# Optimization experiments

Hardware: AMD Instinct MI355X
Metric: run time of the kernel (lower is better)

The kernel has to match this reference:

```python
import jax, jax.numpy as jnp
import numpy as np

EPS = 1e-5
NO_ACT = 3

def _causal_conv(x, w, b, dil):
    # x: [B, Cin, T], w: [Cout, Cin, K]; left-pad by (K-1)*dil == Conv1d(pad)+Chomp1d
    pad = (w.shape[2] - 1) * dil
    y = jax.lax.conv_general_dilated(x, w, window_strides=(1,), padding=[(pad, 0)],
                                     rhs_dilation=(dil,), dimension_numbers=("NCH", "OIH", "NCH"))
    return y + b[None, :, None]

def _bn(x, g, bt, m, v):
    # eval-mode BatchNorm1d over channel dim
    return (x - m[None, :, None]) * (g / jnp.sqrt(v + EPS))[None, :, None] + bt[None, :, None]

def _block(x, w1, b1, w2, b2, g1, bt1, m1, v1, g2, bt2, m2, v2, dil, dw=None, db=None):
    out = jax.nn.relu(_bn(_causal_conv(x, w1, b1, dil), g1, bt1, m1, v1))
    out = jax.nn.relu(_bn(_causal_conv(out, w2, b2, dil), g2, bt2, m2, v2))
    res = x if dw is None else _causal_conv(x, dw, db, 1)
    return jax.nn.relu(out + res)

def _logits(x, c0w1, c0b1, c0w2, c0b2, c0g1, c0bt1, c0m1, c0v1, c0g2, c0bt2, c0m2, c0v2, c0dw, c0db,
            c1w1, c1b1, c1w2, c1b2, c1g1, c1bt1, c1m1, c1v1, c1g2, c1bt2, c1m2, c1v2, aw, ab, lw, lb):
    h = jnp.swapaxes(x, 1, 2)  # [B, Cin, T]
    h = _block(h, c0w1, c0b1, c0w2, c0b2, c0g1, c0bt1, c0m1, c0v1, c0g2, c0bt2, c0m2, c0v2, 1, c0dw, c0db)
    h = _block(h, c1w1, c1b1, c1w2, c1b2, c1g1, c1bt1, c1m1, c1v1, c1g2, c1bt2, c1m2, c1v2, 2)
    z = jnp.swapaxes(h, 1, 2)  # [B, T, C]
    attn = jax.nn.sigmoid(z @ aw + ab)  # [B, T, 1]
    return (z * attn) @ lw + lb  # [B, T, 5]

def setup_inputs():
    key = jax.random.key(0)
    ks = iter(jax.random.split(key, 64))
    B, T, CIN, C, K, NC = 32, 4096, 34, 256, 3, 5
    def conv_w(co, ci, k):
        return jax.random.normal(next(ks), (co, ci, k), jnp.float32) * np.float32(np.sqrt(2.0 / (ci * k)))
    def vec(n, kind="randn"):
        if kind == "randn":
            return jax.random.normal(next(ks), (n,), jnp.float32) * 0.1
        return jax.random.uniform(next(ks), (n,), jnp.float32, 0.5, 1.5)
    inp = {"x": jax.random.normal(next(ks), (B, T, CIN), jnp.float32)}
    for i, ci in [(0, CIN), (1, C)]:
        inp[f"c{i}w1"] = conv_w(C, ci, K); inp[f"c{i}b1"] = vec(C)
        inp[f"c{i}w2"] = conv_w(C, C, K); inp[f"c{i}b2"] = vec(C)
        for j in (1, 2):
            inp[f"c{i}g{j}"] = 1.0 + vec(C)
            inp[f"c{i}bt{j}"] = vec(C)
            inp[f"c{i}m{j}"] = vec(C)
            inp[f"c{i}v{j}"] = vec(C, "rand")
    inp["c0dw"] = conv_w(C, CIN, 1); inp["c0db"] = vec(C)
    inp["aw"] = jax.random.normal(next(ks), (C, 1), jnp.float32) * np.float32(np.sqrt(1.0 / C))
    inp["ab"] = vec(1)
    inp["lw"] = jax.random.normal(next(ks), (C, NC), jnp.float32) * np.float32(np.sqrt(1.0 / C))
    inp["lb"] = vec(NC)
    return inp

def reference(x, c0w1, c0b1, c0w2, c0b2, c0g1, c0bt1, c0m1, c0v1, c0g2, c0bt2, c0m2, c0v2, c0dw, c0db,
              c1w1, c1b1, c1w2, c1b2, c1g1, c1bt1, c1m1, c1v1, c1g2, c1bt2, c1m2, c1v2, aw, ab, lw, lb):
    logits = _logits(x, c0w1, c0b1, c0w2, c0b2, c0g1, c0bt1, c0m1, c0v1, c0g2, c0bt2, c0m2, c0v2, c0dw, c0db,
                     c1w1, c1b1, c1w2, c1b2, c1g1, c1bt1, c1m1, c1v1, c1g2, c1bt2, c1m2, c1v2, aw, ab, lw, lb)
    probs = jax.nn.softmax(logits, axis=-1)
    B, T, NC = probs.shape
    preds = jnp.argmax(probs, axis=-1).astype(jnp.int32)
    # --- conservative no-activity: clipped window (size 5) majority check ---
    non3 = (preds != NO_ACT).astype(jnp.int32)
    cs = jnp.concatenate([jnp.zeros((B, 1), jnp.int32), jnp.cumsum(non3, axis=1)], axis=1)  # [B, T+1]
    t = jnp.arange(T)
    start = jnp.maximum(0, t - 2)
    end = jnp.minimum(T, t + 3)
    wsum = cs[:, end] - cs[:, start]          # non-no-activity count in window, [B, T]
    wlen = (end - start)[None, :]
    alt = jnp.argmax(probs.at[:, :, NO_ACT].set(0.0), axis=-1).astype(jnp.int32)
    proc = jnp.where((preds == NO_ACT) & (2 * wsum > wlen), alt, preds)
    # --- transition rules: sequential state smoothing scan over time ---
    TM = jnp.ones((5, 5), jnp.float32).at[1, 2].set(0.0).at[2, 0].set(0.0)
    def step(prev, inp):
        curr, p = inp                          # curr: [B] int32, p: [B, 5]
        mask = TM[prev]                        # allowed next-states, [B, 5]
        invalid = jnp.take_along_axis(mask, curr[:, None], axis=1)[:, 0] == 0
        vp = p * mask
        cand = jnp.where(vp.sum(-1) == 0, prev, jnp.argmax(vp, axis=-1).astype(jnp.int32))
        new = jnp.where(invalid, cand, curr)
        return new, new
    init = proc[:, 0]
    _, rest = jax.lax.scan(step, init, (proc[:, 1:].T, jnp.swapaxes(probs[:, 1:], 0, 1)))
    processed = jnp.concatenate([init[:, None], rest.T], axis=1)  # [B, T]
    return logits, processed
```

## Files before the change

kernel.cpp:

```cpp
#include <hip/hip_runtime.h>
#include <hip/hip_bf16.h>


#define T_LEN 4096
#define CIN   34
#define EPSV  1e-5f
#define HALO  16
#define TT    48
#define TW    64
#define NTILE 86

__device__ __forceinline__ int hswz(int row, int col) {
    return row * TW + ((((col >> 2) ^ ((row >> 3) & 15)) << 2) | (col & 3));
}
__device__ __forceinline__ float4* lds_ptr4(float* buf, int row, int col) {
    return (float4*)&buf[row * TW + (((col >> 2) ^ ((row >> 3) & 15)) << 2)];
}
__device__ __forceinline__ float4 lds_read4(const float* buf, int row, int col) {
    return *(const float4*)&buf[row * TW + (((col >> 2) ^ ((row >> 3) & 15)) << 2)];
}

__device__ __forceinline__ void bs_load(const float* __restrict__ wraw, int ch,
                                        float4 r[3], int tid) {
    #pragma unroll
    for (int k = 0; k < 3; ++k) {
        int s = tid + k * 512;
        int co = s / 6, q = s - co * 6;
        r[k] = *(const float4*)&wraw[co * 768 + ch * 24 + q * 4];
    }
}
__device__ __forceinline__ void bs_write(float* wch, const float4 r[3], int tid) {
    #pragma unroll
    for (int k = 0; k < 3; ++k) {
        int s = tid + k * 512;
        int co = s / 6, q = s - co * 6;
        wch[(q * 4 + 0) * 256 + co] = r[k].x;
        wch[(q * 4 + 1) * 256 + co] = r[k].y;
        wch[(q * 4 + 2) * 256 + co] = r[k].z;
        wch[(q * 4 + 3) * 256 + co] = r[k].w;
    }
}

__device__ __forceinline__ void s1_load(const float* __restrict__ w1, int ch,
                                        float r[12], int tid) {
    int nrows = (ch < 4) ? 24 : 6;
    int slots = nrows * 256;
    #pragma unroll
    for (int k = 0; k < 12; ++k) {
        int s = tid + k * 512;
        if (s < slots) {
            int co = s / nrows, kr = s - co * nrows;
            r[k] = w1[co * 102 + ch * 24 + kr];
        }
    }
}
__device__ __forceinline__ void s1_write(float* wch, int ch, const float r[12], int tid) {
    int nrows = (ch < 4) ? 24 : 6;
    int slots = nrows * 256;
    #pragma unroll
    for (int k = 0; k < 12; ++k) {
        int s = tid + k * 512;
        if (s < slots) {
            int co = s / nrows, kr = s - co * nrows;
            wch[kr * 256 + co] = r[k];
        }
    }
}

__device__ __forceinline__ void ds_stage(float* wch, const float* __restrict__ dw,
                                         int ch, int tid) {
    int nci = (ch < 4) ? 8 : 2;
    int slots = nci * 256;
    #pragma unroll
    for (int k = 0; k < 4; ++k) {
        int s = tid + k * 512;
        if (s < slots) {
            int ci_l = s % nci, co = s / nci;
            wch[ci_l * 256 + co] = dw[co * CIN + ch * 8 + ci_l];
        }
    }
}

template <int DIL>
__device__ __forceinline__ void chunk_compute(const float* src, const float* wch,
                                              int rowBase, int KH, int co0, int c0,
                                              float (&acc)[8][16]) {
    const int cL = (c0 >= 4) ? c0 - 4 : 0;
    #pragma unroll
    for (int rep = 0; rep < 2; ++rep) {
        int ci_l = KH + rep * 4;
        int row = rowBase + ci_l;
        float rw[20];
        *(float4*)&rw[0]  = lds_read4(src, row, cL);
        *(float4*)&rw[4]  = lds_read4(src, row, c0);
        *(float4*)&rw[8]  = lds_read4(src, row, c0 + 4);
        *(float4*)&rw[12] = lds_read4(src, row, c0 + 8);
        *(float4*)&rw[16] = lds_read4(src, row, c0 + 12);
        #pragma unroll
        for (int kk = 0; kk < 3; ++kk) {
            float wv[8];
            *(float4*)&wv[0] = *(const float4*)&wch[(ci_l * 3 + kk) * 256 + co0];
            *(float4*)&wv[4] = *(const float4*)&wch[(ci_l * 3 + kk) * 256 + co0 + 4];
            const int off = (DIL == 2) ? 2 * kk : kk + 2;
            #pragma unroll
            for (int i = 0; i < 8; ++i)
                #pragma unroll
                for (int j = 0; j < 16; ++j)
                    acc[i][j] += wv[i] * rw[j + off];
        }
    }
}

__device__ __forceinline__ void chunk_compute_x(const float* __restrict__ x,
                                                const float* wch, int b, int t0,
                                                int ciBase, int nci, int KH,
                                                int co0, int c0, float (&acc)[8][16]) {
    #pragma unroll
    for (int rep = 0; rep < 2; ++rep) {
        int ci_l = KH + rep * 4;
        if (ci_l < nci) {
            int ci = ciBase + ci_l;
            float rw[20];
            rw[0] = 0.f; rw[1] = 0.f;
            #pragma unroll
            for (int idx = 2; idx < 20; ++idx) {
                int t = t0 - HALO + c0 + idx - 4;
                rw[idx] = (t >= 0 && t < T_LEN) ? x[(b * T_LEN + t) * CIN + ci] : 0.f;
            }
            #pragma unroll
            for (int kk = 0; kk < 3; ++kk) {
                float wv[8];
                *(float4*)&wv[0] = *(const float4*)&wch[(ci_l * 3 + kk) * 256 + co0];
                *(float4*)&wv[4] = *(const float4*)&wch[(ci_l * 3 + kk) * 256 + co0 + 4];
                #pragma unroll
                for (int i = 0; i < 8; ++i)
                    #pragma unroll
                    for (int j = 0; j < 16; ++j)
                        acc[i][j] += wv[i] * rw[j + kk + 2];
            }
        }
    }
}

__device__ __forceinline__ void chunk_compute_ds(const float* __restrict__ x,
                                                 const float* wch, int b, int t0,
                                                 int ciBase, int nci, int KH,
                                                 int co0, int c0, float (&acc)[8][16]) {
    #pragma unroll
    for (int rep = 0; rep < 2; ++rep) {
        int ci_l = KH + rep * 4;
        if (ci_l < nci) {
            int ci = ciBase + ci_l;
            float xv[16];
            #pragma unroll
            for (int j = 0; j < 16; ++j) {
                int t = t0 - HALO + c0 + j;
                xv[j] = (t >= 0 && t < T_LEN) ? x[(b * T_LEN + t) * CIN + ci] : 0.f;
            }
            float wv[8];
            *(float4*)&wv[0] = *(const float4*)&wch[ci_l * 256 + co0];
            *(float4*)&wv[4] = *(const float4*)&wch[ci_l * 256 + co0 + 4];
            #pragma unroll
            for (int i = 0; i < 8; ++i)
                #pragma unroll
                for (int j = 0; j < 16; ++j)
                    acc[i][j] += wv[i] * xv[j];
        }
    }
}

__device__ __forceinline__ void kh_store(float* tgt, float (&acc)[8][16], int co0, int c0) {
    #pragma unroll
    for (int i = 0; i < 8; ++i)
        #pragma unroll
        for (int j4 = 0; j4 < 4; ++j4)
            *lds_ptr4(tgt, co0 + i, c0 + j4 * 4) =
                make_float4(acc[i][j4*4+0], acc[i][j4*4+1], acc[i][j4*4+2], acc[i][j4*4+3]);
}
__device__ __forceinline__ void kh_add(float* tgt, float (&acc)[8][16], int co0, int c0) {
    #pragma unroll
    for (int i = 0; i < 8; ++i)
        #pragma unroll
        for (int j4 = 0; j4 < 4; ++j4) {
            float4* p = lds_ptr4(tgt, co0 + i, c0 + j4 * 4);
            float4 pv = *p;
            pv.x += acc[i][j4*4+0]; pv.y += acc[i][j4*4+1];
            pv.z += acc[i][j4*4+2]; pv.w += acc[i][j4*4+3];
            *p = pv;
        }
}
__device__ __forceinline__ void kh_final0(float* tgt, float (&acc)[8][16],
                                          const float* __restrict__ g,  const float* __restrict__ bt,
                                          const float* __restrict__ m,  const float* __restrict__ v,
                                          const float* __restrict__ bb,
                                          int co0, int c0, int t0) {
    #pragma unroll
    for (int i = 0; i < 8; ++i) {
        int co = co0 + i;
        float sc = g[co] / sqrtf(v[co] + EPSV);
        float bi = (bb[co] - m[co]) * sc + bt[co];
        #pragma unroll
        for (int j4 = 0; j4 < 4; ++j4) {
            float4* p = lds_ptr4(tgt, co, c0 + j4 * 4);
            float4 pv = *p;
            float pr[4] = {pv.x, pv.y, pv.z, pv.w};
            float o[4];
            #pragma unroll
            for (int r = 0; r < 4; ++r) {
                float s = (pr[r] + acc[i][j4*4+r]) * sc + bi;
                o[r] = fmaxf(s, 0.f);
                int t = t0 - HALO + c0 + j4 * 4 + r;
                if (t < 0) o[r] = 0.f;
            }
            *p = make_float4(o[0], o[1], o[2], o[3]);
        }
    }
}
__device__ __forceinline__ void kh_res2(float* tgt, float (&acc)[8][16],
                                        const float* __restrict__ db,
                                        int co0, int c0, int t0) {
    #pragma unroll
    for (int i = 0; i < 8; ++i) {
        float d = db[co0 + i];
        #pragma unroll
        for (int j4 = 0; j4 < 4; ++j4) {
            float4* p = lds_ptr4(tgt, co0 + i, c0 + j4 * 4);
            float4 pv = *p;
            float pr[4] = {pv.x, pv.y, pv.z, pv.w};
            float o[4];
            #pragma unroll
            for (int r = 0; r < 4; ++r) {
                float s = pr[r] + acc[i][j4*4+r] + d;
                o[r] = fmaxf(s, 0.f);
                int t = t0 - HALO + c0 + j4 * 4 + r;
                if (t < 0) o[r] = 0.f;
            }
            *p = make_float4(o[0], o[1], o[2], o[3]);
        }
    }
}

#define ZERO_ACC() { _Pragma("unroll") for (int i = 0; i < 8; ++i) \
                     _Pragma("unroll") for (int j = 0; j < 16; ++j) acc[i][j] = 0.f; }

#define REDUCE0(TGT, G, BT, M, V, BB) {                         \
    __syncthreads();                                            \
    if (KH == 3) kh_store(TGT, acc, co0, c0);                   \
    __syncthreads();                                            \
    if (KH == 2) kh_add(TGT, acc, co0, c0);                     \
    __syncthreads();                                            \
    if (KH == 1) kh_add(TGT, acc, co0, c0);                     \
    __syncthreads();                                            \
    if (KH == 0) kh_final0(TGT, acc, G, BT, M, V, BB, co0, c0, t0); \
    __syncthreads(); }

#define REDUCE_RES(TGT, DB) {                                   \
    __syncthreads();                                            \
    if (KH == 3) kh_add(TGT, acc, co0, c0);                     \
    __syncthreads();                                            \
    if (KH == 2) kh_add(TGT, acc, co0, c0);                     \
    __syncthreads();                                            \
    if (KH == 1) kh_add(TGT, acc, co0, c0);                     \
    __syncthreads();                                            \
    if (KH == 0) kh_res2(TGT, acc, DB, co0, c0, t0);            \
    __syncthreads(); }

__global__ __launch_bounds__(512, 2) void tcn_fused(
    const float* __restrict__ x,
    const float* __restrict__ c0w1, const float* __restrict__ c0b1,
    const float* __restrict__ c0w2, const float* __restrict__ c0b2,
    const float* __restrict__ c0g1, const float* __restrict__ c0bt1,
    const float* __restrict__ c0m1, const float* __restrict__ c0v1,
    const float* __restrict__ c0g2, const float* __restrict__ c0bt2,
    const float* __restrict__ c0m2, const float* __restrict__ c0v2,
    const float* __restrict__ c1w1, const float* __restrict__ c1b1,
    const float* __restrict__ c1w2, const float* __restrict__ c1b2,
    const float* __restrict__ c1g1, const float* __restrict__ c1bt1,
    const float* __restrict__ c1m1, const float* __restrict__ c1v1,
    const float* __restrict__ c1g2, const float* __restrict__ c1bt2,
    const float* __restrict__ c1m2, const float* __restrict__ c1v2,
    const float* __restrict__ c0dw, const float* __restrict__ c0db,
    const float* __restrict__ aw,   const float* __restrict__ ab,
    const float* __restrict__ lw,   const float* __restrict__ lb,
    float* __restrict__ out)
{
    __shared__ float bufA[256 * TW];
    __shared__ float bufB[256 * TW];
    __shared__ float wch[24 * 256];

    const int b   = blockIdx.y;
    const int t0  = blockIdx.x * TT;
    const int tid = threadIdx.x;
    const int CG  = tid & 31, sg = tid >> 5;
    const int TG  = sg & 3,  KH = sg >> 2;
    const int co0 = CG * 8,  c0 = TG * 16;

    float acc[8][16];

    ZERO_ACC();
    {
        float r[12];
        s1_load(c0w1, 0, r, tid);
        for (int ch = 0; ch < 5; ++ch) {
            __syncthreads();
            s1_write(wch, ch, r, tid);
            __syncthreads();
            if (ch + 1 < 5) s1_load(c0w1, ch + 1, r, tid);
            chunk_compute_x(x, wch, b, t0, ch * 8, (ch < 4) ? 8 : 2, KH, co0, c0, acc);
        }
    }
    REDUCE0(bufA, c0g1, c0bt1, c0m1, c0v1, c0b1);

    ZERO_ACC();
    {
        float4 r4[3];
        bs_load(c0w2, 0, r4, tid);
        for (int ch = 0; ch < 32; ++ch) {
            __syncthreads();
            bs_write(wch, r4, tid);
            __syncthreads();
            if (ch + 1 < 32) bs_load(c0w2, ch + 1, r4, tid);
            chunk_compute<1>(bufA, wch, ch * 8, KH, co0, c0, acc);
        }
    }
    REDUCE0(bufB, c0g2, c0bt2, c0m2, c0v2, c0b2);

    ZERO_ACC();
    for (int ch = 0; ch < 5; ++ch) {
        __syncthreads();
        ds_stage(wch, c0dw, ch, tid);
        __syncthreads();
        chunk_compute_ds(x, wch, b, t0, ch * 8, (ch < 4) ? 8 : 2, KH, co0, c0, acc);
    }
    REDUCE_RES(bufB, c0db);

    ZERO_ACC();
    {
        float4 r4[3];
        bs_load(c1w1, 0, r4, tid);
        for (int ch = 0; ch < 32; ++ch) {
            __syncthreads();
            bs_write(wch, r4, tid);
            __syncthreads();
            if (ch + 1 < 32) bs_load(c1w1, ch + 1, r4, tid);
            chunk_compute<2>(bufB, wch, ch * 8, KH, co0, c0, acc);
        }
    }
    REDUCE0(bufA, c1g1, c1bt1, c1m1, c1v1, c1b1);

    ZERO_ACC();
    {
        float4 r4[3];
        bs_load(c1w2, 0, r4, tid);
        for (int ch = 0; ch < 32; ++ch) {
            __syncthreads();
            bs_write(wch, r4, tid);
            __syncthreads();
            if (ch + 1 < 32) bs_load(c1w2, ch + 1, r4, tid);
            chunk_compute<2>(bufA, wch, ch * 8, KH, co0, c0, acc);
        }
    }
    REDUCE0(bufA, c1g2, c1bt2, c1m2, c1v2, c1b2);

    {
        #pragma unroll
        for (int ii = 0; ii < 2; ++ii) {
            int co = co0 + KH * 2 + ii;
            #pragma unroll
            for (int j4 = 0; j4 < 4; ++j4) {
                float4* p = lds_ptr4(bufA, co, c0 + j4 * 4);
                float4 a = *p;
                float4 rr = lds_read4(bufB, co, c0 + j4 * 4);
                a.x = fmaxf(a.x + rr.x, 0.f);
                a.y = fmaxf(a.y + rr.y, 0.f);
                a.z = fmaxf(a.z + rr.z, 0.f);
                a.w = fmaxf(a.w + rr.w, 0.f);
                *p = a;
            }
        }
    }
    __syncthreads();

    for (int s = tid; s < 1542; s += 512) {
        float vput;
        if (s < 256)       vput = aw[s];
        else if (s < 1536) vput = lw[s - 256];
        else if (s == 1536) vput = ab[0];
        else               vput = lb[s - 1537];
        wch[s] = vput;
    }
    __syncthreads();
    {
        int col = tid >> 3, oct = tid & 7;
        if (col >= HALO) {
            int t = t0 - HALO + col;
            float s1 = 0.f, s5[5] = {0.f, 0.f, 0.f, 0.f, 0.f};
            for (int q = 0; q < 32; ++q) {
                int co = oct * 32 + q;
                float z = bufA[hswz(co, col)];
                s1 += z * wch[co];
                #pragma unroll
                for (int nc = 0; nc < 5; ++nc) s5[nc] += z * wch[256 + co * 5 + nc];
            }
            #pragma unroll
            for (int mm = 1; mm <= 4; mm <<= 1) {
                s1 += __shfl_xor(s1, mm, 64);
                #pragma unroll
                for (int nc = 0; nc < 5; ++nc) s5[nc] += __shfl_xor(s5[nc], mm, 64);
            }
            if (oct == 0 && t < T_LEN) {
                float at = 1.f / (1.f + expf(-(s1 + wch[1536])));
                float* dst = &out[(b * T_LEN + t) * 5];
                #pragma unroll
                for (int nc = 0; nc < 5; ++nc) dst[nc] = at * s5[nc] + wch[1537 + nc];
            }
        }
    }
}

__global__ __launch_bounds__(256) void postproc(
    const float* __restrict__ logits, float* __restrict__ outp)
{
    const int b = blockIdx.x;
    const int tid = threadIdx.x;
    __shared__ signed char preds[4096], alt3[4096], ax2[4096], ax0[4096],
                           proc[4096], resa[4096];

    for (int t = tid; t < T_LEN; t += 256) {
        const float* p = &logits[(b * T_LEN + t) * 5];
        float l0 = p[0], l1 = p[1], l2 = p[2], l3 = p[3], l4 = p[4];
        int am = 0; float mv = l0;
        if (l1 > mv) { am = 1; mv = l1; }
        if (l2 > mv) { am = 2; mv = l2; }
        if (l3 > mv) { am = 3; mv = l3; }
        if (l4 > mv) { am = 4; mv = l4; }
        int a3 = 0; float m3 = l0;
        if (l1 > m3) { a3 = 1; m3 = l1; }
        if (l2 > m3) { a3 = 2; m3 = l2; }
        if (l4 > m3) { a3 = 4; }
        int a2 = 0; float m2 = l0;
        if (l1 > m2) { a2 = 1; m2 = l1; }
        if (l3 > m2) { a2 = 3; m2 = l3; }
        if (l4 > m2) { a2 = 4; }
        int a0 = 1; float m0 = l1;
        if (l2 > m0) { a0 = 2; m0 = l2; }
        if (l3 > m0) { a0 = 3; m0 = l3; }
        if (l4 > m0) { a0 = 4; }
        preds[t] = (signed char)am;
        alt3[t]  = (signed char)a3;
        ax2[t]   = (signed char)a2;
        ax0[t]   = (signed char)a0;
    }
    __syncthreads();
    for (int t = tid; t < T_LEN; t += 256) {
        int s0 = t - 2 > 0 ? t - 2 : 0;
        int e0 = t + 3 < T_LEN ? t + 3 : T_LEN;
        int wsum = 0;
        for (int s = s0; s < e0; ++s) wsum += (preds[s] != 3);
        int wl = e0 - s0;
        int pd = preds[t];
        proc[t] = (pd == 3 && 2 * wsum > wl) ? alt3[t] : (signed char)pd;
    }
    __syncthreads();
    if (tid == 0) {
        int p = proc[0];
        resa[0] = (signed char)p;
        for (int t = 1; t < T_LEN; ++t) {
            int c = proc[t];
            int n = c;
            if (p == 1 && c == 2) n = ax2[t];
            else if (p == 2 && c == 0) n = ax0[t];
            resa[t] = (signed char)n;
            p = n;
        }
    }
    __syncthreads();
    for (int t = tid; t < T_LEN; t += 256) outp[b * T_LEN + t] = (float)resa[t];
}

extern "C" void kernel_launch(void* const* d_in, const int* in_sizes, int n_in,
                              void* d_out, int out_size, void* d_ws, size_t ws_size,
                              hipStream_t stream)
{
    const float* x     = (const float*)d_in[0];
    const float* c0w1  = (const float*)d_in[1];
    const float* c0b1  = (const float*)d_in[2];
    const float* c0w2  = (const float*)d_in[3];
    const float* c0b2  = (const float*)d_in[4];
    const float* c0g1  = (const float*)d_in[5];
    const float* c0bt1 = (const float*)d_in[6];
    const float* c0m1  = (const float*)d_in[7];
    const float* c0v1  = (const float*)d_in[8];
    const float* c0g2  = (const float*)d_in[9];
    const float* c0bt2 = (const float*)d_in[10];
    const float* c0m2  = (const float*)d_in[11];
    const float* c0v2  = (const float*)d_in[12];
    const float* c1w1  = (const float*)d_in[13];
    const float* c1b1  = (const float*)d_in[14];
    const float* c1w2  = (const float*)d_in[15];
    const float* c1b2  = (const float*)d_in[16];
    const float* c1g1  = (const float*)d_in[17];
    const float* c1bt1 = (const float*)d_in[18];
    const float* c1m1  = (const float*)d_in[19];
    const float* c1v1  = (const float*)d_in[20];
    const float* c1g2  = (const float*)d_in[21];
    const float* c1bt2 = (const float*)d_in[22];
    const float* c1m2  = (const float*)d_in[23];
    const float* c1v2  = (const float*)d_in[24];
    const float* c0dw  = (const float*)d_in[25];
    const float* c0db  = (const float*)d_in[26];
    const float* aw    = (const float*)d_in[27];
    const float* ab    = (const float*)d_in[28];
    const float* lw    = (const float*)d_in[29];
    const float* lb    = (const float*)d_in[30];

    float* logits = (float*)d_out;

    tcn_fused<<<dim3(NTILE, 32), 512, 0, stream>>>(
        x,
        c0w1, c0b1, c0w2, c0b2,
        c0g1, c0bt1, c0m1, c0v1,
        c0g2, c0bt2, c0m2, c0v2,
        c1w1, c1b1, c1w2, c1b2,
        c1g1, c1bt1, c1m1, c1v1,
        c1g2, c1bt2, c1m2, c1v2,
        c0dw, c0db, aw, ab, lw, lb,
        logits);

    postproc<<<32, 256, 0, stream>>>(logits, ((float*)d_out) + 32 * 4096 * 5);
}
```

Before: 5.066 ms.

## Add prep kernel for transposed weights and 1024-thread fused TCN reading weights from global

A prep kernel transposes all conv weights into a [ci*3+kk][co] layout in the workspace. A new fused kernel then uses 1024 threads, each computing a 4x4 output block, and reads weights straight from global/L2 instead of staging them in LDS. It keeps the activation tile in LDS and splits each channel sweep into four strided partial sums. The intent is to remove the LDS weight staging, the cross-thread LDS reduction barriers and register pressure, at the cost of more global weight traffic and an extra launch.

```diff
diff --git a/kernel.cpp b/kernel.cpp
--- a/kernel.cpp
+++ b/kernel.cpp
@@ -10,6 +10,13 @@
 #define TW    64
 #define NTILE 86
 
+#define WOFF_WT1 0
+#define WOFF_WT2 26112
+#define WOFF_WT3 222720
+#define WOFF_WT4 419328
+#define WOFF_WTD 615936
+#define WS_FLOATS 624640
+
 __device__ __forceinline__ int hswz(int row, int col) {
     return row * TW + ((((col >> 2) ^ ((row >> 3) & 15)) << 2) | (col & 3));
 }
@@ -18,6 +25,301 @@
 }
 __device__ __forceinline__ float4 lds_read4(const float* buf, int row, int col) {
     return *(const float4*)&buf[row * TW + (((col >> 2) ^ ((row >> 3) & 15)) << 2)];
+}
+
+__global__ __launch_bounds__(256) void prep_v3(
+    const float* __restrict__ c0w1, const float* __restrict__ c0w2,
+    const float* __restrict__ c1w1, const float* __restrict__ c1w2,
+    const float* __restrict__ c0dw, float* __restrict__ ws)
+{
+    int idx = blockIdx.x * 256 + threadIdx.x;
+    if (idx < 26112) {
+        int co = idx & 255, r = idx >> 8, ci = r / 3, kk = r % 3;
+        ws[WOFF_WT1 + idx] = c0w1[(co * CIN + ci) * 3 + kk];
+        return;
+    }
+    idx -= 26112;
+    if (idx < 196608) {
+        int co = idx & 255, r = idx >> 8, ci = r / 3, kk = r % 3;
+        ws[WOFF_WT2 + idx] = c0w2[(co * 256 + ci) * 3 + kk];
+        return;
+    }
+    idx -= 196608;
+    if (idx < 196608) {
+        int co = idx & 255, r = idx >> 8, ci = r / 3, kk = r % 3;
+        ws[WOFF_WT3 + idx] = c1w1[(co * 256 + ci) * 3 + kk];
+        return;
+    }
+    idx -= 196608;
+    if (idx < 196608) {
+        int co = idx & 255, r = idx >> 8, ci = r / 3, kk = r % 3;
+        ws[WOFF_WT4 + idx] = c1w2[(co * 256 + ci) * 3 + kk];
+        return;
+    }
+    idx -= 196608;
+    if (idx < 8704) {
+        int co = idx & 255, ci = idx >> 8;
+        ws[WOFF_WTD + idx] = c0dw[co * CIN + ci];
+    }
+}
+
+__device__ __forceinline__ void bzero(float (&bk)[4][4]) {
+    #pragma unroll
+    for (int i = 0; i < 4; ++i)
+        #pragma unroll
+        for (int j = 0; j < 4; ++j) bk[i][j] = 0.f;
+}
+__device__ __forceinline__ void badd(float (&A)[4][4], const float (&B)[4][4]) {
+    #pragma unroll
+    for (int i = 0; i < 4; ++i)
+        #pragma unroll
+        for (int j = 0; j < 4; ++j) A[i][j] = A[i][j] + B[i][j];
+}
+
+__device__ __forceinline__ void sweep_s1(const float* xs, const float* __restrict__ WT,
+                                         int r, int c0, int co0, float (&bk)[4][4]) {
+    bzero(bk);
+    for (int ci = r; ci < CIN; ci += 4) {
+        float rw[6];
+        #pragma unroll
+        for (int q = 0; q < 6; ++q) rw[q] = xs[ci * 69 + c0 + 2 + q];
+        #pragma unroll
+        for (int kk = 0; kk < 3; ++kk) {
+            float wv[4];
+            *(float4*)&wv[0] = *(const float4*)&WT[(ci * 3 + kk) * 256 + co0];
+            #pragma unroll
+            for (int i = 0; i < 4; ++i)
+                #pragma unroll
+                for (int j = 0; j < 4; ++j)
+                    bk[i][j] += wv[i] * rw[j + kk];
+        }
+    }
+}
+
+template <int DIL>
+__device__ __forceinline__ void sweep_cv(const float* bufH, const float* __restrict__ WT,
+                                         int r, int c0, int cL, int co0, float (&bk)[4][4]) {
+    bzero(bk);
+    for (int ci = r; ci < 256; ci += 4) {
+        float rw[8];
+        *(float4*)&rw[0] = lds_read4(bufH, ci, cL);
+        *(float4*)&rw[4] = lds_read4(bufH, ci, c0);
+        #pragma unroll
+        for (int kk = 0; kk < 3; ++kk) {
+            float wv[4];
+            *(float4*)&wv[0] = *(const float4*)&WT[(ci * 3 + kk) * 256 + co0];
+            const int off = (DIL == 2) ? 2 * kk : kk + 2;
+            #pragma unroll
+            for (int i = 0; i < 4; ++i)
+                #pragma unroll
+                for (int j = 0; j < 4; ++j)
+                    bk[i][j] += wv[i] * rw[j + off];
+        }
+    }
+}
+
+__device__ __forceinline__ void sweep_ds(const float* xs, const float* __restrict__ WTD,
+                                         int r, int c0, int co0, float (&bk)[4][4]) {
+    bzero(bk);
+    for (int ci = r; ci < CIN; ci += 4) {
+        float xv[4];
+        #pragma unroll
+        for (int q = 0; q < 4; ++q) xv[q] = xs[ci * 69 + c0 + 4 + q];
+        float wv[4];
+        *(float4*)&wv[0] = *(const float4*)&WTD[ci * 256 + co0];
+        #pragma unroll
+        for (int i = 0; i < 4; ++i)
+            #pragma unroll
+            for (int j = 0; j < 4; ++j)
+                bk[i][j] += wv[i] * xv[j];
+    }
+}
+
+__global__ __launch_bounds__(1024, 4) void tcn_v4(
+    const float* __restrict__ x,  const float* __restrict__ ws,
+    const float* __restrict__ c0b1, const float* __restrict__ c0g1,
+    const float* __restrict__ c0bt1, const float* __restrict__ c0m1, const float* __restrict__ c0v1,
+    const float* __restrict__ c0b2, const float* __restrict__ c0g2,
+    const float* __restrict__ c0bt2, const float* __restrict__ c0m2, const float* __restrict__ c0v2,
+    const float* __restrict__ c1b1, const float* __restrict__ c1g1,
+    const float* __restrict__ c1bt1, const float* __restrict__ c1m1, const float* __restrict__ c1v1,
+    const float* __restrict__ c1b2, const float* __restrict__ c1g2,
+    const float* __restrict__ c1bt2, const float* __restrict__ c1m2, const float* __restrict__ c1v2,
+    const float* __restrict__ c0db,
+    const float* __restrict__ aw, const float* __restrict__ ab,
+    const float* __restrict__ lw, const float* __restrict__ lb,
+    float* __restrict__ out)
+{
+    __shared__ float bufH[256 * TW];
+    __shared__ float xs[34 * 69];
+
+    const int b   = blockIdx.y;
+    const int t0  = blockIdx.x * TT;
+    const int tid = threadIdx.x;
+    const int CG  = tid >> 4, TG = tid & 15;
+    const int co0 = CG * 4,  c0 = TG * 4;
+    const int cL  = (c0 >= 4) ? c0 - 4 : 0;
+
+    const float* WT1 = ws + WOFF_WT1;
+    const float* WT2 = ws + WOFF_WT2;
+    const float* WT3 = ws + WOFF_WT3;
+    const float* WT4 = ws + WOFF_WT4;
+    const float* WTD = ws + WOFF_WTD;
+
+    for (int s = tid; s < 34 * 68; s += 1024) {
+        int ci = s % 34, col = s / 34;
+        int t = t0 - 20 + col;
+        xs[ci * 69 + col] = (t >= 0 && t < T_LEN) ? x[(b * T_LEN + t) * CIN + ci] : 0.f;
+    }
+    __syncthreads();
+
+    float B1[4][4], B2[4][4], hr[4][4], ot[4][4];
+
+    sweep_s1(xs, WT1, 3, c0, co0, B1);
+    sweep_s1(xs, WT1, 2, c0, co0, B2); badd(B1, B2);
+    sweep_s1(xs, WT1, 1, c0, co0, B2); badd(B1, B2);
+    sweep_s1(xs, WT1, 0, c0, co0, B2);
+    #pragma unroll
+    for (int i = 0; i < 4; ++i) {
+        int co = co0 + i;
+        float sc = c0g1[co] / sqrtf(c0v1[co] + EPSV);
+        float bi = (c0b1[co] - c0m1[co]) * sc + c0bt1[co];
+        float o[4];
+        #pragma unroll
+        for (int j = 0; j < 4; ++j) {
+            float s = (B1[i][j] + B2[i][j]) * sc + bi;
+            float ov = fmaxf(s, 0.f);
+            int t = t0 - HALO + c0 + j;
+            if (t < 0) ov = 0.f;
+            o[j] = ov;
+        }
+        *lds_ptr4(bufH, co, c0) = make_float4(o[0], o[1], o[2], o[3]);
+    }
+    __syncthreads();
+
+    sweep_cv<1>(bufH, WT2, 3, c0, cL, co0, B1);
+    sweep_cv<1>(bufH, WT2, 2, c0, cL, co0, B2); badd(B1, B2);
+    sweep_cv<1>(bufH, WT2, 1, c0, cL, co0, B2); badd(B1, B2);
+    sweep_cv<1>(bufH, WT2, 0, c0, cL, co0, B2);
+    #pragma unroll
+    for (int i = 0; i < 4; ++i) {
+        int co = co0 + i;
+        float sc = c0g2[co] / sqrtf(c0v2[co] + EPSV);
+        float bi = (c0b2[co] - c0m2[co]) * sc + c0bt2[co];
+        #pragma unroll
+        for (int j = 0; j < 4; ++j) {
+            float s = (B1[i][j] + B2[i][j]) * sc + bi;
+            float ov = fmaxf(s, 0.f);
+            int t = t0 - HALO + c0 + j;
+            if (t < 0) ov = 0.f;
+            hr[i][j] = ov;
+        }
+    }
+    sweep_ds(xs, WTD, 3, c0, co0, B1); badd(hr, B1);
+    sweep_ds(xs, WTD, 2, c0, co0, B1); badd(hr, B1);
+    sweep_ds(xs, WTD, 1, c0, co0, B1); badd(hr, B1);
+    sweep_ds(xs, WTD, 0, c0, co0, B1);
+    #pragma unroll
+    for (int i = 0; i < 4; ++i) {
+        float d = c0db[co0 + i];
+        #pragma unroll
+        for (int j = 0; j < 4; ++j) {
+            float s = hr[i][j] + B1[i][j] + d;
+            float ov = fmaxf(s, 0.f);
+            int t = t0 - HALO + c0 + j;
+            if (t < 0) ov = 0.f;
+            hr[i][j] = ov;
+        }
+    }
+    __syncthreads();
+    #pragma unroll
+    for (int i = 0; i < 4; ++i)
+        *lds_ptr4(bufH, co0 + i, c0) = make_float4(hr[i][0], hr[i][1], hr[i][2], hr[i][3]);
+    __syncthreads();
+
+    sweep_cv<2>(bufH, WT3, 3, c0, cL, co0, B1);
+    sweep_cv<2>(bufH, WT3, 2, c0, cL, co0, B2); badd(B1, B2);
+    sweep_cv<2>(bufH, WT3, 1, c0, cL, co0, B2); badd(B1, B2);
+    sweep_cv<2>(bufH, WT3, 0, c0, cL, co0, B2);
+    #pragma unroll
+    for (int i = 0; i < 4; ++i) {
+        int co = co0 + i;
+        float sc = c1g1[co] / sqrtf(c1v1[co] + EPSV);
+        float bi = (c1b1[co] - c1m1[co]) * sc + c1bt1[co];
+        #pragma unroll
+        for (int j = 0; j < 4; ++j) {
+            float s = (B1[i][j] + B2[i][j]) * sc + bi;
+            float ov = fmaxf(s, 0.f);
+            int t = t0 - HALO + c0 + j;
+            if (t < 0) ov = 0.f;
+            ot[i][j] = ov;
+        }
+    }
+    __syncthreads();
+    #pragma unroll
+    for (int i = 0; i < 4; ++i)
+        *lds_ptr4(bufH, co0 + i, c0) = make_float4(ot[i][0], ot[i][1], ot[i][2], ot[i][3]);
+    __syncthreads();
+
+    sweep_cv<2>(bufH, WT4, 3, c0, cL, co0, B1);
+    sweep_cv<2>(bufH, WT4, 2, c0, cL, co0, B2); badd(B1, B2);
+    sweep_cv<2>(bufH, WT4, 1, c0, cL, co0, B2); badd(B1, B2);
+    sweep_cv<2>(bufH, WT4, 0, c0, cL, co0, B2);
+    #pragma unroll
+    for (int i = 0; i < 4; ++i) {
+        int co = co0 + i;
+        float sc = c1g2[co] / sqrtf(c1v2[co] + EPSV);
+        float bi = (c1b2[co] - c1m2[co]) * sc + c1bt2[co];
+        #pragma unroll
+        for (int j = 0; j < 4; ++j) {
+            float s = (B1[i][j] + B2[i][j]) * sc + bi;
+            float a = fmaxf(s, 0.f);
+            int t = t0 - HALO + c0 + j;
+            if (t < 0) a = 0.f;
+            ot[i][j] = fmaxf(a + hr[i][j], 0.f);
+        }
+    }
+    __syncthreads();
+    #pragma unroll
+    for (int i = 0; i < 4; ++i)
+        *lds_ptr4(bufH, co0 + i, c0) = make_float4(ot[i][0], ot[i][1], ot[i][2], ot[i][3]);
+    __syncthreads();
+
+    for (int s = tid; s < 1542; s += 1024) {
+        float vput;
+        if (s < 256)        vput = aw[s];
+        else if (s < 1536)  vput = lw[s - 256];
+        else if (s == 1536) vput = ab[0];
+        else                vput = lb[s - 1537];
+        xs[s] = vput;
+    }
+    __syncthreads();
+    if (tid < 512) {
+        int col = tid >> 3, oct = tid & 7;
+        if (col >= HALO) {
+            int t = t0 - HALO + col;
+            float s1 = 0.f, s5[5] = {0.f, 0.f, 0.f, 0.f, 0.f};
+            for (int q = 0; q < 32; ++q) {
+                int co = oct * 32 + q;
+                float z = bufH[hswz(co, col)];
+                s1 += z * xs[co];
+                #pragma unroll
+                for (int nc = 0; nc < 5; ++nc) s5[nc] += z * xs[256 + co * 5 + nc];
+            }
+            #pragma unroll
+            for (int mm = 1; mm <= 4; mm <<= 1) {
+                s1 += __shfl_xor(s1, mm, 64);
+                #pragma unroll
+                for (int nc = 0; nc < 5; ++nc) s5[nc] += __shfl_xor(s5[nc], mm, 64);
+            }
+            if (oct == 0 && t < T_LEN) {
+                float at = 1.f / (1.f + expf(-(s1 + xs[1536])));
+                float* dst = &out[(b * T_LEN + t) * 5];
+                #pragma unroll
+                for (int nc = 0; nc < 5; ++nc) dst[nc] = at * s5[nc] + xs[1537 + nc];
+            }
+        }
+    }
 }
 
 __device__ __forceinline__ void bs_load(const float* __restrict__ wraw, int ch,
@@ -40,7 +342,6 @@
         wch[(q * 4 + 3) * 256 + co] = r[k].w;
     }
 }
-
 __device__ __forceinline__ void s1_load(const float* __restrict__ w1, int ch,
                                         float r[12], int tid) {
     int nrows = (ch < 4) ? 24 : 6;
@@ -66,7 +367,6 @@
         }
     }
 }
-
 __device__ __forceinline__ void ds_stage(float* wch, const float* __restrict__ dw,
                                          int ch, int tid) {
     int nci = (ch < 4) ? 8 : 2;
@@ -80,18 +380,17 @@
         }
     }
 }
-
 template <int DIL>
 __device__ __forceinline__ void chunk_compute(const float* src, const float* wch,
                                               int rowBase, int KH, int co0, int c0,
                                               float (&acc)[8][16]) {
-    const int cL = (c0 >= 4) ? c0 - 4 : 0;
+    const int cLx = (c0 >= 4) ? c0 - 4 : 0;
     #pragma unroll
     for (int rep = 0; rep < 2; ++rep) {
         int ci_l = KH + rep * 4;
         int row = rowBase + ci_l;
         float rw[20];
-        *(float4*)&rw[0]  = lds_read4(src, row, cL);
+        *(float4*)&rw[0]  = lds_read4(src, row, cLx);
         *(float4*)&rw[4]  = lds_read4(src, row, c0);
         *(float4*)&rw[8]  = lds_read4(src, row, c0 + 4);
         *(float4*)&rw[12] = lds_read4(src, row, c0 + 8);
@@ -110,7 +409,6 @@
         }
     }
 }
-
 __device__ __forceinline__ void chunk_compute_x(const float* __restrict__ x,
                                                 const float* wch, int b, int t0,
                                                 int ciBase, int nci, int KH,
@@ -141,7 +439,6 @@
         }
     }
 }
-
 __device__ __forceinline__ void chunk_compute_ds(const float* __restrict__ x,
                                                  const float* wch, int b, int t0,
                                                  int ciBase, int nci, int KH,
@@ -168,7 +465,6 @@
         }
     }
 }
-
 __device__ __forceinline__ void kh_store(float* tgt, float (&acc)[8][16], int co0, int c0) {
     #pragma unroll
     for (int i = 0; i < 8; ++i)
@@ -239,10 +535,8 @@
         }
     }
 }
-
 #define ZERO_ACC() { _Pragma("unroll") for (int i = 0; i < 8; ++i) \
                      _Pragma("unroll") for (int j = 0; j < 16; ++j) acc[i][j] = 0.f; }
-
 #define REDUCE0(TGT, G, BT, M, V, BB) {                         \
     __syncthreads();                                            \
     if (KH == 3) kh_store(TGT, acc, co0, c0);                   \
@@ -253,7 +547,6 @@
     __syncthreads();                                            \
     if (KH == 0) kh_final0(TGT, acc, G, BT, M, V, BB, co0, c0, t0); \
     __syncthreads(); }
-
 #define REDUCE_RES(TGT, DB) {                                   \
     __syncthreads();                                            \
     if (KH == 3) kh_add(TGT, acc, co0, c0);                     \
@@ -516,16 +809,28 @@
 
     float* logits = (float*)d_out;
 
-    tcn_fused<<<dim3(NTILE, 32), 512, 0, stream>>>(
-        x,
-        c0w1, c0b1, c0w2, c0b2,
-        c0g1, c0bt1, c0m1, c0v1,
-        c0g2, c0bt2, c0m2, c0v2,
-        c1w1, c1b1, c1w2, c1b2,
-        c1g1, c1bt1, c1m1, c1v1,
-        c1g2, c1bt2, c1m2, c1v2,
-        c0dw, c0db, aw, ab, lw, lb,
-        logits);
+    if (ws_size >= (size_t)WS_FLOATS * 4) {
+        float* ws = (float*)d_ws;
+        prep_v3<<<2440, 256, 0, stream>>>(c0w1, c0w2, c1w1, c1w2, c0dw, ws);
+        tcn_v4<<<dim3(NTILE, 32), 1024, 0, stream>>>(
+            x, ws,
+            c0b1, c0g1, c0bt1, c0m1, c0v1,
+            c0b2, c0g2, c0bt2, c0m2, c0v2,
+            c1b1, c1g1, c1bt1, c1m1, c1v1,
+            c1b2, c1g2, c1bt2, c1m2, c1v2,
+            c0db, aw, ab, lw, lb, logits);
+    } else {
+        tcn_fused<<<dim3(NTILE, 32), 512, 0, stream>>>(
+            x,
+            c0w1, c0b1, c0w2, c0b2,
+            c0g1, c0bt1, c0m1, c0v1,
+            c0g2, c0bt2, c0m2, c0v2,
+            c1w1, c1b1, c1w2, c1b2,
+            c1g1, c1bt1, c1m1, c1v1,
+            c1g2, c1bt2, c1m2, c1v2,
+            c0dw, c0db, aw, ab, lw, lb,
+            logits);
+    }
 
     postproc<<<32, 256, 0, stream>>>(logits, ((float*)d_out) + 32 * 4096 * 5);
 }
```

Result: faster. 4.284 ms (-15.4%).
